# Performance work log

Hardware: AMD Instinct MI355X
Metric: run time of the kernel (lower is better)

Reference implementation:

```python
import jax, jax.numpy as jnp
import numpy as np

L = 9  # local window size


def local_windows(x, l):
    # x: (n, c, h, w) -> (n, c, l*l, h, w): all l*l shifted views (zero-padded),
    # equivalent to F.unfold(x, kernel=(l,l), stride=1, padding=l//2).
    n, c, h, w = x.shape
    pad = l // 2
    xp = jnp.pad(x, ((0, 0), (0, 0), (pad, pad), (pad, pad)))
    views = [xp[:, :, i:i + h, j:j + w] for i in range(l) for j in range(l)]
    return jnp.stack(views, axis=2)


def setup_inputs() -> dict:
    key = jax.random.key(0)
    k1, k2, k3 = jax.random.split(key, 3)
    n, c, h, w = 2, 128, 64, 64
    ft = jax.random.normal(k1, (n, c, h, w), dtype=jnp.float32)
    fk = jax.random.normal(k2, (n, c, h, w), dtype=jnp.float32)
    # 1x1 conv weight shared between key and query projections: (out_c, in_c)
    W = jax.random.normal(k3, (128, 128), dtype=jnp.float32) * (1.0 / np.sqrt(128))
    return {"ft": ft, "fk": fk, "W": W}


def reference(ft, fk, W):
    # 1x1 conv == channel matmul
    key = jnp.einsum('oi,nihw->nohw', W, ft)    # key from frame t
    query = jnp.einsum('oi,nihw->nohw', W, fk)  # query from frame k
    # f_similar(query, key, L): per-pixel query dotted with L*L local keys
    key_win = local_windows(key, L)             # (n, c, L*L, h, w)
    sim = jnp.einsum('nchw,nckhw->nhwk', query, key_win)  # (n, h, w, L*L)
    weight = jax.nn.softmax(sim, axis=-1)
    # f_weighting(ft, weight, L): weighted sum of L*L local raw-ft vectors
    ft_win = local_windows(ft, L)                # (n, c, L*L, h, w)
    out = jnp.einsum('nckhw,nhwk->nchw', ft_win, weight)
    return out
```

## Files before the change

kernel.cpp:

```cpp
#include <hip/hip_runtime.h>
#include <hip/hip_bf16.h>


#define Hh 64
#define Ww 64
#define Cc 128
#define Nn 2
#define KK 81
#define HW (Hh * Ww)
#define CHW (Cc * HW)
#define P_TOT (Nn * HW)

typedef _Float16 h8 __attribute__((ext_vector_type(8)));
typedef _Float16 h4 __attribute__((ext_vector_type(4)));
typedef float f4v __attribute__((ext_vector_type(4)));

__global__ __launch_bounds__(256) void proj_kernel(const float* __restrict__ ft,
                                                   const float* __restrict__ fk,
                                                   const float* __restrict__ Wm,
                                                   _Float16* __restrict__ Qbuf,
                                                   _Float16* __restrict__ Kbuf,
                                                   _Float16* __restrict__ fth) {
    __shared__ __align__(16) _Float16 Wth[128 * 136];
    __shared__ __align__(16) _Float16 xkh[32 * 136];
    __shared__ __align__(16) _Float16 xqh[32 * 136];
    const int t = threadIdx.x;
    const int p0 = blockIdx.x * 32;
    const int nn = p0 >> 12;
    const int gbase = nn * CHW + (p0 & 4095);

#pragma unroll 4
    for (int e = t; e < 4096; e += 256) {
        const int n = e >> 5, ch = e & 31;
        const float4 v = *(const float4*)&Wm[n * 128 + (ch << 2)];
        h4 hv; hv[0] = (_Float16)v.x; hv[1] = (_Float16)v.y;
               hv[2] = (_Float16)v.z; hv[3] = (_Float16)v.w;
        *(h4*)&Wth[n * 136 + (ch << 2)] = hv;
    }
#pragma unroll 4
    for (int e = t; e < 1024; e += 256) {
        const int c = e >> 3, pc = e & 7;
        const float4 vk = *(const float4*)&ft[gbase + c * HW + (pc << 2)];
        const float4 vq = *(const float4*)&fk[gbase + c * HW + (pc << 2)];
        const int px = pc << 2;
        xkh[(px    ) * 136 + c] = (_Float16)vk.x;
        xkh[(px + 1) * 136 + c] = (_Float16)vk.y;
        xkh[(px + 2) * 136 + c] = (_Float16)vk.z;
        xkh[(px + 3) * 136 + c] = (_Float16)vk.w;
        xqh[(px    ) * 136 + c] = (_Float16)vq.x;
        xqh[(px + 1) * 136 + c] = (_Float16)vq.y;
        xqh[(px + 2) * 136 + c] = (_Float16)vq.z;
        xqh[(px + 3) * 136 + c] = (_Float16)vq.w;
    }
    __syncthreads();

#pragma unroll
    for (int e = t; e < 512; e += 256) {
        const int px = e >> 4, cq = e & 15;
        *(h8*)&fth[(size_t)(p0 + px) * 128 + (cq << 3)] =
            *(const h8*)&xkh[px * 136 + (cq << 3)];
    }

    const int lane = t & 63, wv = t >> 6;
    const int quad = lane >> 4, l15 = lane & 15;
    const _Float16* xs = (wv >> 1) ? xqh : xkh;
    _Float16* dst = (wv >> 1) ? Qbuf : Kbuf;
    const int mt = wv & 1;
    const int abase = (mt * 16 + l15) * 136 + (quad << 3);
    const h8 a0 = *(const h8*)&xs[abase];
    const h8 a1 = *(const h8*)&xs[abase + 32];
    const h8 a2 = *(const h8*)&xs[abase + 64];
    const h8 a3 = *(const h8*)&xs[abase + 96];
#pragma unroll
    for (int nt = 0; nt < 8; ++nt) {
        const int bbase = (nt * 16 + l15) * 136 + (quad << 3);
        const h8 b0 = *(const h8*)&Wth[bbase];
        const h8 b1 = *(const h8*)&Wth[bbase + 32];
        const h8 b2 = *(const h8*)&Wth[bbase + 64];
        const h8 b3 = *(const h8*)&Wth[bbase + 96];
        f4v acc = {0.f, 0.f, 0.f, 0.f};
        acc = __builtin_amdgcn_mfma_f32_16x16x32_f16(a0, b0, acc, 0, 0, 0);
        acc = __builtin_amdgcn_mfma_f32_16x16x32_f16(a1, b1, acc, 0, 0, 0);
        acc = __builtin_amdgcn_mfma_f32_16x16x32_f16(a2, b2, acc, 0, 0, 0);
        acc = __builtin_amdgcn_mfma_f32_16x16x32_f16(a3, b3, acc, 0, 0, 0);
        const int col = nt * 16 + l15;
        const size_t rb = (size_t)(p0 + mt * 16 + (quad << 2)) * 128 + col;
#pragma unroll
        for (int r = 0; r < 4; ++r)
            dst[rb + (size_t)r * 128] = (_Float16)acc[r];
    }
}

__global__ __launch_bounds__(256, 4) void sim_weight_kernel(const _Float16* __restrict__ Qbuf,
                                                            const _Float16* __restrict__ Kbuf,
                                                            const _Float16* __restrict__ fth,
                                                            float* __restrict__ out) {
    __shared__ __align__(16) unsigned char smem[40720];
    _Float16* Ksw  = (_Float16*)smem;
    _Float16* Qsw  = (_Float16*)(smem + 36864);
    _Float16* ftl  = (_Float16*)smem;
    float*    simbF= (float*)smem;
    _Float16* simb = (_Float16*)(smem + 39168);
    float*    redM = (float*)(smem + 40464);
    float*    redS = (float*)(smem + 40592);

    const int t  = threadIdx.x;
    const int b  = blockIdx.x;
    const int x0 = (b & 7) << 3;
    const int y  = (b >> 3) & 63;
    const int nn = b >> 9;
    const int pg0 = (nn << 12) + (y << 6) + x0;

#pragma unroll 3
    for (int e = t; e < 144 * 16; e += 256) {
        const int v = e >> 4, ci = e & 15;
        const int gx = x0 + (v & 15) - 4;
        const int gy = y + (v >> 4) - 4;
        h8 val = {0, 0, 0, 0, 0, 0, 0, 0};
        if ((unsigned)gx < 64u && (unsigned)gy < 64u)
            val = *(const h8*)&Kbuf[(size_t)((nn << 12) + (gy << 6) + gx) * 128 + (ci << 3)];
        *(h8*)&Ksw[(v << 7) + ((ci ^ (v & 15)) << 3)] = val;
    }
    if (t < 128) {
        const int v = t >> 4, ci = t & 15;
        *(h8*)&Qsw[(v << 7) + ((ci ^ v) << 3)] =
            *(const h8*)&Qbuf[(size_t)(pg0 + v) * 128 + (ci << 3)];
    }
    __syncthreads();

    const int lane = t & 63, wv = t >> 6;
    const int quad = lane >> 4, l15 = lane & 15;
    const int qrow = l15 & 7;
    h8 qb[4];
#pragma unroll
    for (int kc = 0; kc < 4; ++kc) {
        const int ci = (kc << 2) + quad;
        qb[kc] = *(const h8*)&Qsw[(qrow << 7) + ((ci ^ qrow) << 3)];
    }
    const int r0 = wv, r1 = wv + 4;
    f4v acc0 = {0.f,0.f,0.f,0.f}, acc1 = acc0, acc2 = acc0;
#pragma unroll
    for (int kc = 0; kc < 4; ++kc) {
        const int ci = (kc << 2) + quad;
        const h8 kA = *(const h8*)&Ksw[(((r0 << 4) + l15) << 7) + ((ci ^ l15) << 3)];
        const h8 kB = *(const h8*)&Ksw[(((r1 << 4) + l15) << 7) + ((ci ^ l15) << 3)];
        const h8 kC = *(const h8*)&Ksw[(((8  << 4) + l15) << 7) + ((ci ^ l15) << 3)];
        acc0 = __builtin_amdgcn_mfma_f32_16x16x32_f16(kA, qb[kc], acc0, 0, 0, 0);
        acc1 = __builtin_amdgcn_mfma_f32_16x16x32_f16(kB, qb[kc], acc1, 0, 0, 0);
        acc2 = __builtin_amdgcn_mfma_f32_16x16x32_f16(kC, qb[kc], acc2, 0, 0, 0);
    }
    __syncthreads();

#pragma unroll
    for (int reg = 0; reg < 4; ++reg) {
        const int xx = (quad << 2) + reg;
        const int dx = xx - l15;
        const bool ok = (l15 < 8) && (dx >= 0) && (dx < 9);
        if (ok)            simbF[(r0 * 9 + dx) * 8 + l15] = acc0[reg];
        if (ok)            simbF[(r1 * 9 + dx) * 8 + l15] = acc1[reg];
        if (ok && wv == 0) simbF[(8  * 9 + dx) * 8 + l15] = acc2[reg];
    }
    __syncthreads();

    const int p = t & 7, kb = t >> 3;
    const bool has2 = (kb + 64 < KK);
    const float s0 = simbF[kb * 8 + p];
    const float s1 = simbF[(kb + 32) * 8 + p];
    const float s2 = has2 ? simbF[(kb + 64) * 8 + p] : 0.f;
    __syncthreads();

#pragma unroll 3
    for (int e = t; e < 144 * 16; e += 256) {
        const int v = e >> 4, ci = e & 15;
        const int gx = x0 + (v & 15) - 4;
        const int gy = y + (v >> 4) - 4;
        h8 val = {0, 0, 0, 0, 0, 0, 0, 0};
        if ((unsigned)gx < 64u && (unsigned)gy < 64u)
            val = *(const h8*)&fth[(size_t)((nn << 12) + (gy << 6) + gx) * 128 + (ci << 3)];
        *(h8*)&ftl[v * 136 + (ci << 3)] = val;
    }

    float m = fmaxf(s0, s1);
    if (has2) m = fmaxf(m, s2);
#pragma unroll
    for (int off = 8; off <= 32; off <<= 1) m = fmaxf(m, __shfl_xor(m, off));
    if ((t & 56) == 0) redM[((t >> 6) << 3) + p] = m;
    __syncthreads();
    float mm = fmaxf(fmaxf(redM[p], redM[8 + p]), fmaxf(redM[16 + p], redM[24 + p]));
    const float e0 = __expf(s0 - mm);
    const float e1 = __expf(s1 - mm);
    const float e2 = has2 ? __expf(s2 - mm) : 0.f;
    simb[kb * 8 + p] = (_Float16)e0;
    simb[(kb + 32) * 8 + p] = (_Float16)e1;
    if (has2) simb[(kb + 64) * 8 + p] = (_Float16)e2;
    float s = e0 + e1 + e2;
#pragma unroll
    for (int off = 8; off <= 32; off <<= 1) s += __shfl_xor(s, off);
    if ((t & 56) == 0) redS[((t >> 6) << 3) + p] = s;
    __syncthreads();
    const float inv = 1.f / (redS[p] + redS[8 + p] + redS[16 + p] + redS[24 + p]);

    const int cq = t >> 3;
    float4 acc = make_float4(0, 0, 0, 0);
    for (int r = 0; r < 9; ++r) {
        const int rb = ((r << 4) + p) * 136 + (cq << 2);
        const int k9 = r * 9;
#pragma unroll
        for (int dx = 0; dx < 9; ++dx) {
            const float w = (float)simb[(k9 + dx) * 8 + p];
            const h4 f = *(const h4*)&ftl[rb + dx * 136];
            acc.x += (float)f[0] * w;
            acc.y += (float)f[1] * w;
            acc.z += (float)f[2] * w;
            acc.w += (float)f[3] * w;
        }
    }
    const size_t ob = (size_t)((nn * Cc + (cq << 2)) << 12) + (y << 6) + x0 + p;
    out[ob]          = acc.x * inv;
    out[ob + HW]     = acc.y * inv;
    out[ob + 2*HW]   = acc.z * inv;
    out[ob + 3*HW]   = acc.w * inv;
}

extern "C" void kernel_launch(void* const* d_in, const int* in_sizes, int n_in,
                              void* d_out, int out_size, void* d_ws, size_t ws_size,
                              hipStream_t stream) {
    const float* ft = (const float*)d_in[0];
    const float* fk = (const float*)d_in[1];
    const float* Wm = (const float*)d_in[2];
    float* out = (float*)d_out;

    _Float16* wsh  = (_Float16*)d_ws;
    _Float16* Qbuf = wsh;
    _Float16* Kbuf = wsh + 1048576;
    _Float16* fth  = wsh + 2097152;

    proj_kernel<<<256, 256, 0, stream>>>(ft, fk, Wm, Qbuf, Kbuf, fth);
    sim_weight_kernel<<<1024, 256, 0, stream>>>(Qbuf, Kbuf, fth, out);
}
```

Before: 79.21 us.

## Swizzle ft tile layout, repack softmax weights per pixel, vectorize projection staging

```diff
diff --git a/kernel.cpp b/kernel.cpp
--- a/kernel.cpp
+++ b/kernel.cpp
@@ -37,20 +37,26 @@
                hv[2] = (_Float16)v.z; hv[3] = (_Float16)v.w;
         *(h4*)&Wth[n * 136 + (ch << 2)] = hv;
     }
-#pragma unroll 4
-    for (int e = t; e < 1024; e += 256) {
-        const int c = e >> 3, pc = e & 7;
-        const float4 vk = *(const float4*)&ft[gbase + c * HW + (pc << 2)];
-        const float4 vq = *(const float4*)&fk[gbase + c * HW + (pc << 2)];
-        const int px = pc << 2;
-        xkh[(px    ) * 136 + c] = (_Float16)vk.x;
-        xkh[(px + 1) * 136 + c] = (_Float16)vk.y;
-        xkh[(px + 2) * 136 + c] = (_Float16)vk.z;
-        xkh[(px + 3) * 136 + c] = (_Float16)vk.w;
-        xqh[(px    ) * 136 + c] = (_Float16)vq.x;
-        xqh[(px + 1) * 136 + c] = (_Float16)vq.y;
-        xqh[(px + 2) * 136 + c] = (_Float16)vq.z;
-        xqh[(px + 3) * 136 + c] = (_Float16)vq.w;
+    {
+        const int pc = t & 7, cg = t >> 3;
+        const int c0 = cg << 2, px0 = pc << 2;
+        float4 vk[4], vq[4];
+#pragma unroll
+        for (int j = 0; j < 4; ++j) {
+            vk[j] = *(const float4*)&ft[gbase + (c0 + j) * HW + px0];
+            vq[j] = *(const float4*)&fk[gbase + (c0 + j) * HW + px0];
+        }
+#pragma unroll
+        for (int pp = 0; pp < 4; ++pp) {
+            h4 hk, hq;
+#pragma unroll
+            for (int j = 0; j < 4; ++j) {
+                hk[j] = (_Float16)((const float*)&vk[j])[pp];
+                hq[j] = (_Float16)((const float*)&vq[j])[pp];
+            }
+            *(h4*)&xkh[(px0 + pp) * 136 + c0] = hk;
+            *(h4*)&xqh[(px0 + pp) * 136 + c0] = hq;
+        }
     }
     __syncthreads();
 
@@ -95,14 +101,14 @@
                                                             const _Float16* __restrict__ Kbuf,
                                                             const _Float16* __restrict__ fth,
                                                             float* __restrict__ out) {
-    __shared__ __align__(16) unsigned char smem[40720];
+    __shared__ __align__(16) unsigned char smem[39552];
     _Float16* Ksw  = (_Float16*)smem;
     _Float16* Qsw  = (_Float16*)(smem + 36864);
     _Float16* ftl  = (_Float16*)smem;
     float*    simbF= (float*)smem;
-    _Float16* simb = (_Float16*)(smem + 39168);
-    float*    redM = (float*)(smem + 40464);
-    float*    redS = (float*)(smem + 40592);
+    _Float16* simb_p=(_Float16*)(smem + 36864);
+    float*    redM = (float*)(smem + 39296);
+    float*    redS = (float*)(smem + 39424);
 
     const int t  = threadIdx.x;
     const int b  = blockIdx.x;
@@ -177,7 +183,7 @@
         h8 val = {0, 0, 0, 0, 0, 0, 0, 0};
         if ((unsigned)gx < 64u && (unsigned)gy < 64u)
             val = *(const h8*)&fth[(size_t)((nn << 12) + (gy << 6) + gx) * 128 + (ci << 3)];
-        *(h8*)&ftl[v * 136 + (ci << 3)] = val;
+        *(h8*)&ftl[(v << 7) + ((ci ^ (v & 15)) << 3)] = val;
     }
 
     float m = fmaxf(s0, s1);
@@ -190,9 +196,12 @@
     const float e0 = __expf(s0 - mm);
     const float e1 = __expf(s1 - mm);
     const float e2 = has2 ? __expf(s2 - mm) : 0.f;
-    simb[kb * 8 + p] = (_Float16)e0;
-    simb[(kb + 32) * 8 + p] = (_Float16)e1;
-    if (has2) simb[(kb + 64) * 8 + p] = (_Float16)e2;
+    {
+        const int k1 = kb + 32, k2 = kb + 64;
+        simb_p[p * 152 + (kb / 9) * 16 + (kb % 9)] = (_Float16)e0;
+        simb_p[p * 152 + (k1 / 9) * 16 + (k1 % 9)] = (_Float16)e1;
+        if (has2) simb_p[p * 152 + (k2 / 9) * 16 + (k2 % 9)] = (_Float16)e2;
+    }
     float s = e0 + e1 + e2;
 #pragma unroll
     for (int off = 8; off <= 32; off <<= 1) s += __shfl_xor(s, off);
@@ -201,14 +210,18 @@
     const float inv = 1.f / (redS[p] + redS[8 + p] + redS[16 + p] + redS[24 + p]);
 
     const int cq = t >> 3;
+    const int ci = cq >> 1, sub = (cq & 1) << 2;
+    const int pb = p * 152;
     float4 acc = make_float4(0, 0, 0, 0);
     for (int r = 0; r < 9; ++r) {
-        const int rb = ((r << 4) + p) * 136 + (cq << 2);
-        const int k9 = r * 9;
+        const h8 wA = *(const h8*)&simb_p[pb + (r << 4)];
+        const float w8 = (float)simb_p[pb + (r << 4) + 8];
+        const int vb = (r << 4) + p;
 #pragma unroll
         for (int dx = 0; dx < 9; ++dx) {
-            const float w = (float)simb[(k9 + dx) * 8 + p];
-            const h4 f = *(const h4*)&ftl[rb + dx * 136];
+            const float w = (dx < 8) ? (float)wA[dx] : w8;
+            const int v = vb + dx;
+            const h4 f = *(const h4*)&ftl[(v << 7) + ((ci ^ (p + dx)) << 3) + sub];
             acc.x += (float)f[0] * w;
             acc.y += (float)f[1] * w;
             acc.z += (float)f[2] * w;
```

Result: no change. 79.92 us (+0.9%).
